# Kernel tuning notes

Measured on AMD Instinct MI355X. Metric: run time of the kernel, lower is better.

## Reference

```python
import jax, jax.numpy as jnp
import numpy as np

B, D_IN, D_H = 1024, 4096, 4096


def setup_inputs() -> dict:
    key = jax.random.key(0)
    ks = jax.random.split(key, 11)
    s_i = 1.0 / np.sqrt(0.5 * (D_IN + D_H))  # xavier_normal std for i2h
    s_h = 1.0 / np.sqrt(D_H)                 # xavier_normal std for h2h
    inp = {
        "x": jax.random.normal(ks[0], (B, D_IN), jnp.float32),
        "h_prev": jax.random.normal(ks[1], (B, D_H), jnp.float32),
        "c_prev": jax.random.normal(ks[2], (B, D_H), jnp.float32),
        "Wi": jax.random.normal(ks[3], (D_IN, D_H), jnp.float32) * s_i,
        "Ui": jax.random.normal(ks[4], (D_H, D_H), jnp.float32) * s_h,
        "bi": jnp.zeros((D_H,), jnp.float32),
        "Wf": jax.random.normal(ks[5], (D_IN, D_H), jnp.float32) * s_i,
        "Uf": jax.random.normal(ks[6], (D_H, D_H), jnp.float32) * s_h,
        "bf": jnp.zeros((D_H,), jnp.float32),
        "Wg": jax.random.normal(ks[7], (D_IN, D_H), jnp.float32) * s_i,
        "Ug": jax.random.normal(ks[8], (D_H, D_H), jnp.float32) * s_h,
        "bg": jnp.zeros((D_H,), jnp.float32),
        "Wo": jax.random.normal(ks[9], (D_IN, D_H), jnp.float32) * s_i,
        "Uo": jax.random.normal(ks[10], (D_H, D_H), jnp.float32) * s_h,
        "bo": jnp.zeros((D_H,), jnp.float32),
    }
    return inp


def reference(x, h_prev, c_prev, Wi, Ui, bi, Wf, Uf, bf, Wg, Ug, bg, Wo, Uo, bo):
    # Fuse the 8 small GEMMs into 2 by concatenating weights along the output dim.
    W = jnp.concatenate([Wi, Wf, Wg, Wo], axis=1)   # [D_IN, 4*D_H]
    U = jnp.concatenate([Ui, Uf, Ug, Uo], axis=1)   # [D_H, 4*D_H]
    b = jnp.concatenate([bi, bf, bg, bo], axis=0)   # [4*D_H]
    z = x @ W + h_prev @ U + b                      # [B, 4*D_H]
    zi, zf, zg, zo = jnp.split(z, 4, axis=1)
    ig = jax.nn.sigmoid(zi)
    fg = jax.nn.sigmoid(zf)
    cc = jnp.tanh(zg)
    og = jax.nn.sigmoid(zo)
    c = fg * c_prev + ig * cc
    h = og * jnp.tanh(c)
    return (h, c)
```

## Files before the change

kernel.cpp:

```cpp
#include <hip/hip_runtime.h>
#include <cstdint>
#include <cstddef>


typedef __bf16 bf16;
typedef __bf16 bf16x8 __attribute__((ext_vector_type(8)));
typedef __bf16 bf16x4 __attribute__((ext_vector_type(4)));
typedef float f32x4 __attribute__((ext_vector_type(4)));

static constexpr int Bn = 1024;
static constexpr int DH = 4096;
static constexpr int K  = 8192;
static constexpr int BM = 512, BN = 64, BK = 32;

__device__ __forceinline__ void load_lds16(const void* g, void* l) {
  __builtin_amdgcn_global_load_lds(
      (const __attribute__((address_space(1))) unsigned int*)g,
      (__attribute__((address_space(3))) unsigned int*)l, 16, 0, 0);
}

__global__ void pack_A(const float* __restrict__ x, const float* __restrict__ h,
                       bf16* __restrict__ A) {
  int idx4 = blockIdx.x * blockDim.x + threadIdx.x;
  int b = idx4 >> 11;
  int q = idx4 & 2047;
  int k = q << 2;
  const float* src = (k < DH) ? (x + (size_t)b * DH + k)
                              : (h + (size_t)b * DH + (k - DH));
  float4 v = *(const float4*)src;
  bf16x4 o;
  o[0] = (bf16)v.x; o[1] = (bf16)v.y; o[2] = (bf16)v.z; o[3] = (bf16)v.w;
  *(bf16x4*)(A + (size_t)idx4 * 4) = o;
}

__global__ __launch_bounds__(256) void conv_w4(
    const float* __restrict__ Wi, const float* __restrict__ Ui,
    const float* __restrict__ Wf, const float* __restrict__ Uf,
    const float* __restrict__ Wg, const float* __restrict__ Ug,
    const float* __restrict__ Wo, const float* __restrict__ Uo,
    bf16* __restrict__ Bt) {
  __shared__ short tile[256 * 66];
  const int bz = blockIdx.z;
  const int gate = bz >> 1, isU = bz & 1;
  const float* src;
  switch (bz) {
    case 0: src = Wi; break; case 1: src = Ui; break;
    case 2: src = Wf; break; case 3: src = Uf; break;
    case 4: src = Wg; break; case 5: src = Ug; break;
    default: src = (bz == 6) ? Wo : Uo; break;
  }
  const int kb = blockIdx.x * 256, n0 = blockIdx.y * 256;
  const int t = threadIdx.x;
  const int c  = t & 63;
  const int rp = t >> 6;
  const int u  = t & 7;
  const int r2 = t >> 3;

  for (int it = 0; it < 4; ++it) {
    const int kt = kb + it * 64;
#pragma unroll
    for (int p = 0; p < 8; ++p) {
      const int kk = p * 4 + rp;
      const int kl = 2 * kk;
      float4 v0 = *(const float4*)(src + (size_t)(kt + kl) * DH + n0 + c * 4);
      float4 v1 = *(const float4*)(src + (size_t)(kt + kl + 1) * DH + n0 + c * 4);
#pragma unroll
      for (int j = 0; j < 4; ++j) {
        bf16 lo = (bf16)((&v0.x)[j]);
        bf16 hi = (bf16)((&v1.x)[j]);
        short2 pk;
        pk.x = __builtin_bit_cast(short, lo);
        pk.y = __builtin_bit_cast(short, hi);
        *(short2*)&tile[(c * 4 + j) * 66 + kk * 2] = pk;
      }
    }
    __syncthreads();
#pragma unroll
    for (int p = 0; p < 8; ++p) {
      const int nl = p * 32 + r2;
      const int* pp = (const int*)&tile[nl * 66 + u * 8];
      int4 o;
      o.x = pp[0]; o.y = pp[1]; o.z = pp[2]; o.w = pp[3];
      const int hc = n0 + nl;
      const size_t row = (size_t)((hc >> 4) * 64 + gate * 16 + (hc & 15));
      *(int4*)(Bt + row * K + (size_t)(isU * DH + kt + 8 * u)) = o;
    }
    __syncthreads();
  }
}

__device__ __forceinline__ float sigm(float x) { return 1.0f / (1.0f + __expf(-x)); }
__device__ __forceinline__ float tanh_(float x) { return 1.0f - 2.0f / (__expf(2.0f * x) + 1.0f); }

__global__ __launch_bounds__(256, 2) void lstm_gemm(
    const bf16* __restrict__ A, const bf16* __restrict__ Bt,
    const float* __restrict__ cp,
    const float* __restrict__ bi, const float* __restrict__ bfv,
    const float* __restrict__ bg, const float* __restrict__ bo,
    float* __restrict__ out) {
  __shared__ __align__(16) bf16 As[BM * BK];
  __shared__ __align__(16) bf16 Bs[BN * BK];
  const int n0 = blockIdx.x * BN;
  const int m0 = blockIdx.y * BM;
  const int t = threadIdx.x, l = t & 63, w = t >> 6;
  const int lane15 = l & 15, quad = l >> 4;
  const int srow = l >> 2;
  const int sg = (l & 3) ^ ((l >> 3) & 3);
  const int fsw = quad ^ ((lane15 >> 1) & 3);

  f32x4 acc[8][4];
#pragma unroll
  for (int i = 0; i < 8; ++i)
#pragma unroll
    for (int j = 0; j < 4; ++j) acc[i][j] = (f32x4)0.0f;

  for (int kt = 0; kt < K / BK; ++kt) {
    const int k0 = kt * BK;
#pragma unroll
    for (int cc = 0; cc < 8; ++cc) {
      const int bb = w * 8 + cc;
      load_lds16(A + (size_t)(m0 + bb * 16 + srow) * K + k0 + sg * 8,
                 (char*)As + bb * 1024);
    }
    load_lds16(Bt + (size_t)(n0 + w * 16 + srow) * K + k0 + sg * 8,
               (char*)Bs + w * 1024);
    __syncthreads();
    bf16x8 aF[8], bF[4];
#pragma unroll
    for (int i = 0; i < 8; ++i)
      aF[i] = *(const bf16x8*)((const char*)As + ((w * 8 + i) << 10) +
                               (lane15 << 6) + (fsw << 4));
#pragma unroll
    for (int j = 0; j < 4; ++j)
      bF[j] = *(const bf16x8*)((const char*)Bs + (j << 10) +
                               (lane15 << 6) + (fsw << 4));
#pragma unroll
    for (int i = 0; i < 8; ++i)
#pragma unroll
      for (int j = 0; j < 4; ++j)
        acc[i][j] = __builtin_amdgcn_mfma_f32_16x16x32_bf16(aF[i], bF[j], acc[i][j], 0, 0, 0);
    __syncthreads();
  }

  const int hc = blockIdx.x * 16 + lane15;
  const float vbi = bi[hc], vbf = bfv[hc], vbg = bg[hc], vbo = bo[hc];
  float* outh = out;
  float* outc = out + (size_t)Bn * DH;
#pragma unroll
  for (int i = 0; i < 8; ++i) {
    const int brow = m0 + w * 128 + i * 16 + quad * 4;
#pragma unroll
    for (int r = 0; r < 4; ++r) {
      const int b = brow + r;
      const float zi = acc[i][0][r] + vbi;
      const float zf = acc[i][1][r] + vbf;
      const float zg = acc[i][2][r] + vbg;
      const float zo = acc[i][3][r] + vbo;
      const float ig = sigm(zi), fg = sigm(zf), gg = tanh_(zg), og = sigm(zo);
      const float cprev = cp[(size_t)b * DH + hc];
      const float cnew = fg * cprev + ig * gg;
      outh[(size_t)b * DH + hc] = og * tanh_(cnew);
      outc[(size_t)b * DH + hc] = cnew;
    }
  }
}

extern "C" void kernel_launch(void* const* d_in, const int* in_sizes, int n_in,
                              void* d_out, int out_size, void* d_ws, size_t ws_size,
                              hipStream_t stream) {
  const float* x  = (const float*)d_in[0];
  const float* hp = (const float*)d_in[1];
  const float* cp = (const float*)d_in[2];
  const float* Wi = (const float*)d_in[3];
  const float* Ui = (const float*)d_in[4];
  const float* bi = (const float*)d_in[5];
  const float* Wf = (const float*)d_in[6];
  const float* Uf = (const float*)d_in[7];
  const float* bf = (const float*)d_in[8];
  const float* Wg = (const float*)d_in[9];
  const float* Ug = (const float*)d_in[10];
  const float* bg = (const float*)d_in[11];
  const float* Wo = (const float*)d_in[12];
  const float* Uo = (const float*)d_in[13];
  const float* bo = (const float*)d_in[14];

  bf16* Aw = (bf16*)d_ws;
  bf16* Bt = (bf16*)((char*)d_ws + ((size_t)16 << 20));

  hipLaunchKernelGGL(conv_w4, dim3(16, 16, 8), dim3(256), 0, stream,
                     Wi, Ui, Wf, Uf, Wg, Ug, Wo, Uo, Bt);
  hipLaunchKernelGGL(pack_A, dim3((Bn * K / 4) / 256), dim3(256), 0, stream, x, hp, Aw);
  hipLaunchKernelGGL(lstm_gemm, dim3((4 * DH) / BN, Bn / BM), dim3(256), 0, stream,
                     Aw, Bt, cp, bi, bf, bg, bo, (float*)d_out);
}
```

Before: 879.2 us.

## Fuse fp32 weight conversion into GEMM and double-buffer LDS tiles

Drops the separate conv_w4 pass that transposed and converted all eight fp32 weight matrices to a packed bf16 buffer. The GEMM now reads fp32 weights directly, converts them in registers and writes them into a swizzled LDS layout. It also double-buffers both the A and B tiles so the next k-step's loads overlap the current MFMAs, with one barrier per iteration. This saves a 512MB-read/256MB-write pre-pass, but each GEMM block reads fp32 weights (twice the bytes of bf16), only two blocks along M share them, and LDS use doubles to about 72KB.

```diff
diff --git a/kernel.cpp b/kernel.cpp
--- a/kernel.cpp
+++ b/kernel.cpp
@@ -12,6 +12,10 @@
 static constexpr int DH = 4096;
 static constexpr int K  = 8192;
 static constexpr int BM = 512, BN = 64, BK = 32;
+static constexpr int NT = K / BK;
+static constexpr int AS_SZ = BM * BK * 2;
+static constexpr int BS_SZ = BN * BK * 2;
+static constexpr int LDS_TOTAL = 2 * AS_SZ + 2 * BS_SZ;
 
 __device__ __forceinline__ void load_lds16(const void* g, void* l) {
   __builtin_amdgcn_global_load_lds(
@@ -33,74 +37,20 @@
   *(bf16x4*)(A + (size_t)idx4 * 4) = o;
 }
 
-__global__ __launch_bounds__(256) void conv_w4(
+__device__ __forceinline__ float sigm(float x) { return 1.0f / (1.0f + __expf(-x)); }
+__device__ __forceinline__ float tanh_(float x) { return 1.0f - 2.0f / (__expf(2.0f * x) + 1.0f); }
+
+__global__ __launch_bounds__(256, 2) void lstm_fused(
+    const bf16* __restrict__ A,
     const float* __restrict__ Wi, const float* __restrict__ Ui,
     const float* __restrict__ Wf, const float* __restrict__ Uf,
     const float* __restrict__ Wg, const float* __restrict__ Ug,
     const float* __restrict__ Wo, const float* __restrict__ Uo,
-    bf16* __restrict__ Bt) {
-  __shared__ short tile[256 * 66];
-  const int bz = blockIdx.z;
-  const int gate = bz >> 1, isU = bz & 1;
-  const float* src;
-  switch (bz) {
-    case 0: src = Wi; break; case 1: src = Ui; break;
-    case 2: src = Wf; break; case 3: src = Uf; break;
-    case 4: src = Wg; break; case 5: src = Ug; break;
-    default: src = (bz == 6) ? Wo : Uo; break;
-  }
-  const int kb = blockIdx.x * 256, n0 = blockIdx.y * 256;
-  const int t = threadIdx.x;
-  const int c  = t & 63;
-  const int rp = t >> 6;
-  const int u  = t & 7;
-  const int r2 = t >> 3;
-
-  for (int it = 0; it < 4; ++it) {
-    const int kt = kb + it * 64;
-#pragma unroll
-    for (int p = 0; p < 8; ++p) {
-      const int kk = p * 4 + rp;
-      const int kl = 2 * kk;
-      float4 v0 = *(const float4*)(src + (size_t)(kt + kl) * DH + n0 + c * 4);
-      float4 v1 = *(const float4*)(src + (size_t)(kt + kl + 1) * DH + n0 + c * 4);
-#pragma unroll
-      for (int j = 0; j < 4; ++j) {
-        bf16 lo = (bf16)((&v0.x)[j]);
-        bf16 hi = (bf16)((&v1.x)[j]);
-        short2 pk;
-        pk.x = __builtin_bit_cast(short, lo);
-        pk.y = __builtin_bit_cast(short, hi);
-        *(short2*)&tile[(c * 4 + j) * 66 + kk * 2] = pk;
-      }
-    }
-    __syncthreads();
-#pragma unroll
-    for (int p = 0; p < 8; ++p) {
-      const int nl = p * 32 + r2;
-      const int* pp = (const int*)&tile[nl * 66 + u * 8];
-      int4 o;
-      o.x = pp[0]; o.y = pp[1]; o.z = pp[2]; o.w = pp[3];
-      const int hc = n0 + nl;
-      const size_t row = (size_t)((hc >> 4) * 64 + gate * 16 + (hc & 15));
-      *(int4*)(Bt + row * K + (size_t)(isU * DH + kt + 8 * u)) = o;
-    }
-    __syncthreads();
-  }
-}
-
-__device__ __forceinline__ float sigm(float x) { return 1.0f / (1.0f + __expf(-x)); }
-__device__ __forceinline__ float tanh_(float x) { return 1.0f - 2.0f / (__expf(2.0f * x) + 1.0f); }
-
-__global__ __launch_bounds__(256, 2) void lstm_gemm(
-    const bf16* __restrict__ A, const bf16* __restrict__ Bt,
     const float* __restrict__ cp,
     const float* __restrict__ bi, const float* __restrict__ bfv,
     const float* __restrict__ bg, const float* __restrict__ bo,
     float* __restrict__ out) {
-  __shared__ __align__(16) bf16 As[BM * BK];
-  __shared__ __align__(16) bf16 Bs[BN * BK];
-  const int n0 = blockIdx.x * BN;
+  extern __shared__ __align__(16) char lds[];
   const int m0 = blockIdx.y * BM;
   const int t = threadIdx.x, l = t & 63, w = t >> 6;
   const int lane15 = l & 15, quad = l >> 4;
@@ -108,37 +58,93 @@
   const int sg = (l & 3) ^ ((l >> 3) & 3);
   const int fsw = quad ^ ((lane15 >> 1) & 3);
 
+  const int p = l >> 2;
+  const int cq = l & 3;
+  const int hcol0 = blockIdx.x * 16;
+  const float* baseW; const float* baseU;
+  switch (w) {
+    case 0: baseW = Wi; baseU = Ui; break;
+    case 1: baseW = Wf; baseU = Uf; break;
+    case 2: baseW = Wg; baseU = Ug; break;
+    default: baseW = Wo; baseU = Uo; break;
+  }
+  baseW += hcol0 + cq * 4;
+  baseU += hcol0 + cq * 4;
+
   f32x4 acc[8][4];
 #pragma unroll
   for (int i = 0; i < 8; ++i)
 #pragma unroll
     for (int j = 0; j < 4; ++j) acc[i][j] = (f32x4)0.0f;
 
-  for (int kt = 0; kt < K / BK; ++kt) {
-    const int k0 = kt * BK;
+  {
+    const float* pb = baseW + (size_t)(2 * p) * DH;
+    float4 v0 = *(const float4*)pb;
+    float4 v1 = *(const float4*)(pb + DH);
 #pragma unroll
     for (int cc = 0; cc < 8; ++cc) {
       const int bb = w * 8 + cc;
-      load_lds16(A + (size_t)(m0 + bb * 16 + srow) * K + k0 + sg * 8,
-                 (char*)As + bb * 1024);
-    }
-    load_lds16(Bt + (size_t)(n0 + w * 16 + srow) * K + k0 + sg * 8,
-               (char*)Bs + w * 1024);
+      load_lds16(A + (size_t)(m0 + bb * 16 + srow) * K + sg * 8,
+                 lds + bb * 1024);
+    }
+#pragma unroll
+    for (int j = 0; j < 4; ++j) {
+      const int np = w * 16 + cq * 4 + j;
+      const int slot = (p >> 2) ^ ((np >> 1) & 3);
+      short2 pk;
+      pk.x = __builtin_bit_cast(short, (bf16)((&v0.x)[j]));
+      pk.y = __builtin_bit_cast(short, (bf16)((&v1.x)[j]));
+      *(short2*)(lds + 2 * AS_SZ + np * 64 + slot * 16 + 4 * (p & 3)) = pk;
+    }
     __syncthreads();
+  }
+
+  for (int kt = 0; kt < NT; ++kt) {
+    const int cur = kt & 1;
+    char* As  = lds + cur * AS_SZ;
+    char* Bs  = lds + 2 * AS_SZ + cur * BS_SZ;
+    char* Asn = lds + (cur ^ 1) * AS_SZ;
+    char* Bsn = lds + 2 * AS_SZ + (cur ^ 1) * BS_SZ;
+    const bool hn = (kt + 1) < NT;
+    float4 v0, v1;
+    if (hn) {
+      const int k0n = (kt + 1) * BK;
+      const int kg = k0n + 2 * p;
+      const float* pb = (kg < DH) ? (baseW + (size_t)kg * DH)
+                                  : (baseU + (size_t)(kg - DH) * DH);
+      v0 = *(const float4*)pb;
+      v1 = *(const float4*)(pb + DH);
+#pragma unroll
+      for (int cc = 0; cc < 8; ++cc) {
+        const int bb = w * 8 + cc;
+        load_lds16(A + (size_t)(m0 + bb * 16 + srow) * K + k0n + sg * 8,
+                   Asn + bb * 1024);
+      }
+    }
     bf16x8 aF[8], bF[4];
 #pragma unroll
     for (int i = 0; i < 8; ++i)
-      aF[i] = *(const bf16x8*)((const char*)As + ((w * 8 + i) << 10) +
+      aF[i] = *(const bf16x8*)(As + ((w * 8 + i) << 10) +
                                (lane15 << 6) + (fsw << 4));
 #pragma unroll
     for (int j = 0; j < 4; ++j)
-      bF[j] = *(const bf16x8*)((const char*)Bs + (j << 10) +
-                               (lane15 << 6) + (fsw << 4));
+      bF[j] = *(const bf16x8*)(Bs + (j << 10) + (lane15 << 6) + (fsw << 4));
 #pragma unroll
     for (int i = 0; i < 8; ++i)
 #pragma unroll
       for (int j = 0; j < 4; ++j)
         acc[i][j] = __builtin_amdgcn_mfma_f32_16x16x32_bf16(aF[i], bF[j], acc[i][j], 0, 0, 0);
+    if (hn) {
+#pragma unroll
+      for (int j = 0; j < 4; ++j) {
+        const int np = w * 16 + cq * 4 + j;
+        const int slot = (p >> 2) ^ ((np >> 1) & 3);
+        short2 pk;
+        pk.x = __builtin_bit_cast(short, (bf16)((&v0.x)[j]));
+        pk.y = __builtin_bit_cast(short, (bf16)((&v1.x)[j]));
+        *(short2*)(Bsn + np * 64 + slot * 16 + 4 * (p & 3)) = pk;
+      }
+    }
     __syncthreads();
   }
 
@@ -185,11 +191,17 @@
   const float* bo = (const float*)d_in[14];
 
   bf16* Aw = (bf16*)d_ws;
-  bf16* Bt = (bf16*)((char*)d_ws + ((size_t)16 << 20));
-
-  hipLaunchKernelGGL(conv_w4, dim3(16, 16, 8), dim3(256), 0, stream,
-                     Wi, Ui, Wf, Uf, Wg, Ug, Wo, Uo, Bt);
+
+  static bool attr_set = false;
+  if (!attr_set) {
+    hipFuncSetAttribute((const void*)lstm_fused,
+                        hipFuncAttributeMaxDynamicSharedMemorySize, LDS_TOTAL);
+    attr_set = true;
+  }
+
   hipLaunchKernelGGL(pack_A, dim3((Bn * K / 4) / 256), dim3(256), 0, stream, x, hp, Aw);
-  hipLaunchKernelGGL(lstm_gemm, dim3((4 * DH) / BN, Bn / BM), dim3(256), 0, stream,
-                     Aw, Bt, cp, bi, bf, bg, bo, (float*)d_out);
-}
+  hipLaunchKernelGGL(lstm_fused, dim3((4 * DH) / BN, Bn / BM), dim3(256),
+                     LDS_TOTAL, stream,
+                     Aw, Wi, Ui, Wf, Uf, Wg, Ug, Wo, Uo,
+                     cp, bi, bf, bg, bo, (float*)d_out);
+}
```

New measurement: 800.6 us. -8.9%, faster.
